# Kernel optimization log

Measured on AMD Instinct MI355X. Metric: run time of the kernel, lower is better.

The kernel has to match this reference:

```python
import jax, jax.numpy as jnp
import numpy as np

B, S, E, H = 4, 2048, 1024, 16
D = E // H  # per-head dim
SCALE = float(1.0 / np.sqrt(D))


def setup_inputs() -> dict:
    key = jax.random.key(0)
    k1, k2, k3 = jax.random.split(key, 3)
    x = jax.random.normal(k1, (B, S, E), dtype=jnp.float32)
    # xavier_uniform for torch Linear weights (shape [out, in])
    lim_qkv = float(np.sqrt(6.0 / (E + 3 * E)))
    w_qkv = jax.random.uniform(k2, (3 * E, E), minval=-lim_qkv, maxval=lim_qkv, dtype=jnp.float32)
    lim_o = float(np.sqrt(6.0 / (E + E)))
    w_o = jax.random.uniform(k3, (E, E), minval=-lim_o, maxval=lim_o, dtype=jnp.float32)
    return {"x": x, "w_qkv": w_qkv, "w_o": w_o}


def reference(x, w_qkv, w_o):
    b, s, e = x.shape
    # self-attention projection: (b,s,3E) -> (b,s,H,3D) -> chunk into q,k,v
    qkv = (x @ w_qkv.T).reshape(b, s, H, 3 * D)
    q, k, v = jnp.split(qkv, 3, axis=-1)           # each (b,s,H,D)
    q = q.transpose(0, 2, 1, 3)                    # (b,H,s,D)
    k = k.transpose(0, 2, 1, 3)
    v = v.transpose(0, 2, 1, 3)
    logits = jnp.einsum("bhsd,bhtd->bhst", q, k) * SCALE  # (b,H,s,s)
    # NOTE: faithful to source bug — values use raw scaled logits, not softmax(logits)
    values = jnp.einsum("bhst,bhtd->bhsd", logits, v)     # (b,H,s,D)
    values = values.transpose(0, 2, 1, 3).reshape(b, s, e)
    return values @ w_o.T
```

## Files before the change

kernel.cpp:

```cpp
#include <hip/hip_runtime.h>
#include <hip/hip_bf16.h>
#include <cstdint>

#define SCALE_F 0.125f

typedef __attribute__((ext_vector_type(8))) short bf16x8;
typedef __attribute__((ext_vector_type(4))) float f32x4;
typedef __attribute__((ext_vector_type(4))) unsigned short u16x4;
typedef __attribute__((ext_vector_type(8))) unsigned short u16x8;

typedef const __attribute__((address_space(1))) void glb_void;
typedef __attribute__((address_space(3))) void lds_void;

static __device__ __forceinline__ unsigned short f2bf(float f) {
  unsigned u = __builtin_bit_cast(unsigned, f);
  u = (u + 0x7fffu + ((u >> 16) & 1u)) >> 16;
  return (unsigned short)u;
}
static __device__ __forceinline__ float bf2f(unsigned short s) {
  unsigned u = ((unsigned)s) << 16;
  return __builtin_bit_cast(float, u);
}

static __device__ __forceinline__ int xcd_work(int bid, int nwg) {
  int cpx = nwg >> 3;
  return (bid & 7) * cpx + (bid >> 3);
}

__global__ __launch_bounds__(256) void prep(const float* __restrict__ x,
                                            const float* __restrict__ wqkv,
                                            const float* __restrict__ wo,
                                            unsigned short* __restrict__ xb,
                                            unsigned short* __restrict__ xT,
                                            unsigned short* __restrict__ wqt,
                                            unsigned short* __restrict__ wk,
                                            unsigned short* __restrict__ wv,
                                            unsigned short* __restrict__ wob) {
  __shared__ unsigned short lds[64][72];
  const int t = threadIdx.x;
  const int bid = blockIdx.x;

  if (bid < 2048) {
    const int r0 = (bid & 127) * 64, c0 = (bid >> 7) * 64;
#pragma unroll
    for (int pass = 0; pass < 4; ++pass) {
      int r = pass * 16 + (t >> 4);
      int c = (t & 15) * 4;
      float4 v = *(const float4*)(x + (size_t)(r0 + r) * 1024 + c0 + c);
      u16x4 o = { f2bf(v.x), f2bf(v.y), f2bf(v.z), f2bf(v.w) };
      *(u16x4*)(xb + (size_t)(r0 + r) * 1024 + c0 + c) = o;
#pragma unroll
      for (int j = 0; j < 4; ++j) {
        int C = c + j;
        lds[C][r ^ ((C & 7) << 3)] = o[j];
      }
    }
    __syncthreads();
#pragma unroll
    for (int pass = 0; pass < 2; ++pass) {
      int rr = pass * 32 + (t >> 3);
      int cc = (t & 7) * 8;
      u16x8 v = *(const u16x8*)&lds[rr][cc ^ ((rr & 7) << 3)];
      *(u16x8*)(xT + (size_t)(c0 + rr) * 8192 + r0 + cc) = v;
    }
  } else if (bid < 5120) {
    int row = bid - 2048;
    const float* src;
    unsigned short* dst;
    if (row < 1024) {
      int h = row >> 6, k = row & 63;
      src = wqkv + (size_t)(h * 192 + 64 + k) * 1024;
      dst = wk + (size_t)row * 1024;
    } else if (row < 2048) {
      int local = row - 1024;
      int h = local >> 6, k = local & 63;
      src = wqkv + (size_t)(h * 192 + 128 + k) * 1024;
      dst = wv + (size_t)local * 1024;
    } else {
      int local = row - 2048;
      src = wo + (size_t)local * 1024;
      dst = wob + (size_t)local * 1024;
    }
    float4 v = *(const float4*)(src + t * 4);
    u16x4 o = { f2bf(v.x), f2bf(v.y), f2bf(v.z), f2bf(v.w) };
    *(u16x4*)(dst + t * 4) = o;
  } else {
    int tid = bid - 5120;
    const int r0 = (tid & 15) * 64, c0 = (tid >> 4) * 64;
#pragma unroll
    for (int pass = 0; pass < 4; ++pass) {
      int r = pass * 16 + (t >> 4);
      int c = (t & 15) * 4;
      int gr = r0 + r;
      int srcRow = (gr >> 6) * 192 + (gr & 63);
      float4 v = *(const float4*)(wqkv + (size_t)srcRow * 1024 + c0 + c);
      lds[c + 0][r] = f2bf(v.x);
      lds[c + 1][r] = f2bf(v.y);
      lds[c + 2][r] = f2bf(v.z);
      lds[c + 3][r] = f2bf(v.w);
    }
    __syncthreads();
#pragma unroll
    for (int pass = 0; pass < 2; ++pass) {
      int rr = pass * 32 + (t >> 3);
      int cc = (t & 7) * 8;
      *(u16x8*)(wqt + (size_t)(c0 + rr) * 1024 + r0 + cc) = *(const u16x8*)&lds[rr][cc];
    }
  }
}

template<bool F32OUT>
__global__ __launch_bounds__(512) void gemm_bt(const unsigned short* __restrict__ A, int lda,
                                               long aB, long aP,
                                               const unsigned short* __restrict__ Bm, int ldb,
                                               long bB, long bP,
                                               void* __restrict__ Cv, int ldc,
                                               long cB, long cP,
                                               int K, int psplit, int nx, int ny) {
  __shared__ __align__(16) unsigned short Ash[2][128 * 32];
  __shared__ __align__(16) unsigned short Bsh[2][128 * 32];
  const int work = xcd_work(blockIdx.x, gridDim.x);
  const int xt = work % nx;
  const int yt = (work / nx) % ny;
  const int z  = work / (nx * ny);
  const int bb = z / psplit, pp = z % psplit;
  A  += (size_t)bb * aB + (size_t)pp * aP;
  Bm += (size_t)bb * bB + (size_t)pp * bP;
  const int t = threadIdx.x;
  const int w = t >> 6, l = t & 63;
  const int lr = l & 15, lk = l >> 4;
  const int m0 = yt * 128, n0 = xt * 128;
  const int wr = (w >> 2) * 64, wc = (w & 3) * 32;
  const int srow = t >> 2;
  const int skc = ((t & 3) ^ ((srow >> 1) & 3)) << 3;
  const size_t aOff = (size_t)(m0 + srow) * lda + skc;
  const size_t bOff = (size_t)(n0 + srow) * ldb + skc;
  const int fxor = ((lk ^ ((lr >> 1) & 3)) << 3);
  f32x4 acc[4][2] = {};

  __builtin_amdgcn_global_load_lds((glb_void*)(A + aOff), (lds_void*)(Ash[0] + w * 512), 16, 0, 0);
  __builtin_amdgcn_global_load_lds((glb_void*)(Bm + bOff), (lds_void*)(Bsh[0] + w * 512), 16, 0, 0);
  __syncthreads();

  int cur = 0;
  for (int k0 = 0; k0 < K; k0 += 32, cur ^= 1) {
    if (k0 + 32 < K) {
      __builtin_amdgcn_global_load_lds((glb_void*)(A + aOff + k0 + 32),
                                       (lds_void*)(Ash[cur ^ 1] + w * 512), 16, 0, 0);
      __builtin_amdgcn_global_load_lds((glb_void*)(Bm + bOff + k0 + 32),
                                       (lds_void*)(Bsh[cur ^ 1] + w * 512), 16, 0, 0);
    }
    bf16x8 af[4], bfv[2];
#pragma unroll
    for (int mi = 0; mi < 4; ++mi)
      af[mi] = *(const bf16x8*)(Ash[cur] + (wr + mi * 16 + lr) * 32 + fxor);
#pragma unroll
    for (int ni = 0; ni < 2; ++ni)
      bfv[ni] = *(const bf16x8*)(Bsh[cur] + (wc + ni * 16 + lr) * 32 + fxor);
#pragma unroll
    for (int mi = 0; mi < 4; ++mi)
#pragma unroll
      for (int ni = 0; ni < 2; ++ni)
        acc[mi][ni] = __builtin_amdgcn_mfma_f32_16x16x32_bf16(af[mi], bfv[ni], acc[mi][ni], 0, 0, 0);
    __syncthreads();
  }

#pragma unroll
  for (int mi = 0; mi < 4; ++mi)
#pragma unroll
    for (int ni = 0; ni < 2; ++ni)
#pragma unroll
      for (int r = 0; r < 4; ++r) {
        const size_t row = (size_t)(m0 + wr + mi * 16 + lk * 4 + r);
        const size_t col = (size_t)(n0 + wc + ni * 16 + lr);
        if constexpr (F32OUT)
          ((float*)Cv)[(size_t)bb * cB + (size_t)pp * cP + row * ldc + col] = acc[mi][ni][r];
        else
          ((unsigned short*)Cv)[(size_t)bb * cB + (size_t)pp * cP + row * ldc + col] = f2bf(acc[mi][ni][r]);
      }
}

__global__ __launch_bounds__(512) void gemm_tri(const unsigned short* __restrict__ xT,
                                                unsigned short* __restrict__ Gp) {
  __shared__ __align__(16) unsigned short Ash[2][128 * 32];
  __shared__ __align__(16) unsigned short Bsh[2][128 * 32];
  const int work = xcd_work(blockIdx.x, gridDim.x);
  int ti = work % 36;
  const int z = work / 36;
  int mt = 0, accum = 0;
  while (accum + mt + 1 <= ti) { accum += mt + 1; ++mt; }
  int nt = ti - accum;
  const int b = z >> 2, p = z & 3;
  const unsigned short* base = xT + (size_t)b * 2048 + (size_t)p * 512;

  const int t = threadIdx.x;
  const int w = t >> 6, l = t & 63;
  const int lr = l & 15, lk = l >> 4;
  const int m0 = mt * 128, n0 = nt * 128;
  const int wr = (w >> 2) * 64, wc = (w & 3) * 32;
  const int srow = t >> 2;
  const int skc = ((t & 3) ^ ((srow >> 1) & 3)) << 3;
  const size_t aOff = (size_t)(m0 + srow) * 8192 + skc;
  const size_t bOff = (size_t)(n0 + srow) * 8192 + skc;
  const int fxor = ((lk ^ ((lr >> 1) & 3)) << 3);
  f32x4 acc[4][2] = {};

  __builtin_amdgcn_global_load_lds((glb_void*)(base + aOff), (lds_void*)(Ash[0] + w * 512), 16, 0, 0);
  __builtin_amdgcn_global_load_lds((glb_void*)(base + bOff), (lds_void*)(Bsh[0] + w * 512), 16, 0, 0);
  __syncthreads();

  int cur = 0;
  for (int k0 = 0; k0 < 512; k0 += 32, cur ^= 1) {
    if (k0 + 32 < 512) {
      __builtin_amdgcn_global_load_lds((glb_void*)(base + aOff + k0 + 32),
                                       (lds_void*)(Ash[cur ^ 1] + w * 512), 16, 0, 0);
      __builtin_amdgcn_global_load_lds((glb_void*)(base + bOff + k0 + 32),
                                       (lds_void*)(Bsh[cur ^ 1] + w * 512), 16, 0, 0);
    }
    bf16x8 af[4], bfv[2];
#pragma unroll
    for (int mi = 0; mi < 4; ++mi)
      af[mi] = *(const bf16x8*)(Ash[cur] + (wr + mi * 16 + lr) * 32 + fxor);
#pragma unroll
    for (int ni = 0; ni < 2; ++ni)
      bfv[ni] = *(const bf16x8*)(Bsh[cur] + (wc + ni * 16 + lr) * 32 + fxor);
#pragma unroll
    for (int mi = 0; mi < 4; ++mi)
#pragma unroll
      for (int ni = 0; ni < 2; ++ni)
        acc[mi][ni] = __builtin_amdgcn_mfma_f32_16x16x32_bf16(af[mi], bfv[ni], acc[mi][ni], 0, 0, 0);
    __syncthreads();
  }

  unsigned short* out = Gp + (size_t)z * 1048576;
#pragma unroll
  for (int mi = 0; mi < 4; ++mi)
#pragma unroll
    for (int ni = 0; ni < 2; ++ni)
#pragma unroll
      for (int r = 0; r < 4; ++r)
        out[(size_t)(m0 + wr + mi * 16 + lk * 4 + r) * 1024 + n0 + wc + ni * 16 + lr]
            = f2bf(acc[mi][ni][r]);
}

__global__ __launch_bounds__(256) void mirror_reduce(const unsigned short* __restrict__ Gp,
                                                     unsigned short* __restrict__ G) {
  __shared__ unsigned short ldsT[128][128];
  int ti = blockIdx.x;
  int mt = 0, accum = 0;
  while (accum + mt + 1 <= ti) { accum += mt + 1; ++mt; }
  int nt = ti - accum;
  const int b = blockIdx.y;
  const int m0 = mt * 128, n0 = nt * 128;
  const unsigned short* base = Gp + (size_t)b * 4 * 1048576;
  unsigned short* Gb = G + (size_t)b * 1048576;
  const int t = threadIdx.x;

#pragma unroll
  for (int pass = 0; pass < 8; ++pass) {
    int idx = pass * 2048 + t * 8;
    int r = idx >> 7, c = idx & 127;
    float s[8] = {};
#pragma unroll
    for (int p = 0; p < 4; ++p) {
      u16x8 v = *(const u16x8*)(base + (size_t)p * 1048576 + (size_t)(m0 + r) * 1024 + n0 + c);
#pragma unroll
      for (int j = 0; j < 8; ++j) s[j] += bf2f(v[j]);
    }
    u16x8 o;
#pragma unroll
    for (int j = 0; j < 8; ++j) o[j] = f2bf(s[j]);
    *(u16x8*)(Gb + (size_t)(m0 + r) * 1024 + n0 + c) = o;
#pragma unroll
    for (int j = 0; j < 8; ++j) {
      int col = c + j;
      ldsT[col][r ^ (((col >> 3) & 7) << 3)] = o[j];
    }
  }

  if (mt != nt) {
    __syncthreads();
#pragma unroll
    for (int pass = 0; pass < 8; ++pass) {
      int idx = pass * 2048 + t * 8;
      int rr = idx >> 7, cc = idx & 127;
      u16x8 v = *(const u16x8*)&ldsT[rr][cc ^ (((rr >> 3) & 7) << 3)];
      *(u16x8*)(Gb + (size_t)(n0 + rr) * 1024 + m0 + cc) = v;
    }
  }
}

__global__ __launch_bounds__(512) void mdirect(const unsigned short* __restrict__ wk,
                                               const unsigned short* __restrict__ G,
                                               const unsigned short* __restrict__ wv,
                                               float* __restrict__ Mp) {
  __shared__ __align__(16) unsigned short Awk[2][64 * 32];
  __shared__ __align__(16) unsigned short Bg[2][128 * 32];
  __shared__ __align__(16) unsigned short Ut[64 * 128];
  __shared__ __align__(16) unsigned short WvS[64 * 128];
  const int work = xcd_work(blockIdx.x, gridDim.x);
  const int bh = work >> 3, es = work & 7;
  const int b = bh >> 4, h = bh & 15;
  const int e0 = es * 128;
  const int t = threadIdx.x;
  const int w = t >> 6, l = t & 63;
  const int lr = l & 15, lk = l >> 4;

  const unsigned short* wkB = wk + (size_t)(h * 64) * 1024;
  const unsigned short* Gb  = G + (size_t)b * 1048576 + (size_t)e0 * 1024;
  const unsigned short* wvB = wv + (size_t)(h * 64) * 1024 + e0;

  const int arow = t >> 2, askc = ((t & 3) ^ ((arow >> 1) & 3)) << 3;
  const int brow = t >> 2, bskc = ((t & 3) ^ ((brow >> 1) & 3)) << 3;
  const size_t aOff = (size_t)arow * 1024 + askc;
  const size_t bOff = (size_t)brow * 1024 + bskc;
  const int fxor = ((lk ^ ((lr >> 1) & 3)) << 3);

#pragma unroll
  for (int i = 0; i < 2; ++i) {
    int idx = i * 512 + t;
    int row = idx >> 4, slot = idx & 15;
    int sslot = slot ^ (row & 15);
    __builtin_amdgcn_global_load_lds(
        (glb_void*)(wvB + (size_t)row * 1024 + sslot * 8),
        (lds_void*)(WvS + i * 4096 + w * 512), 16, 0, 0);
  }
  if (t < 256)
    __builtin_amdgcn_global_load_lds((glb_void*)(wkB + aOff),
                                     (lds_void*)(Awk[0] + w * 512), 16, 0, 0);
  __builtin_amdgcn_global_load_lds((glb_void*)(Gb + bOff),
                                   (lds_void*)(Bg[0] + w * 512), 16, 0, 0);
  __syncthreads();

  const int wc = w * 16;
  f32x4 acc[4] = {};
  int cur = 0;
  for (int k0 = 0; k0 < 1024; k0 += 32, cur ^= 1) {
    if (k0 + 32 < 1024) {
      if (t < 256)
        __builtin_amdgcn_global_load_lds((glb_void*)(wkB + aOff + k0 + 32),
                                         (lds_void*)(Awk[cur ^ 1] + w * 512), 16, 0, 0);
      __builtin_amdgcn_global_load_lds((glb_void*)(Gb + bOff + k0 + 32),
                                       (lds_void*)(Bg[cur ^ 1] + w * 512), 16, 0, 0);
    }
    bf16x8 af[4], bfv;
#pragma unroll
    for (int mi = 0; mi < 4; ++mi)
      af[mi] = *(const bf16x8*)(Awk[cur] + (mi * 16 + lr) * 32 + fxor);
    bfv = *(const bf16x8*)(Bg[cur] + (wc + lr) * 32 + fxor);
#pragma unroll
    for (int mi = 0; mi < 4; ++mi)
      acc[mi] = __builtin_amdgcn_mfma_f32_16x16x32_bf16(af[mi], bfv, acc[mi], 0, 0, 0);
    __syncthreads();
  }

#pragma unroll
  for (int mi = 0; mi < 4; ++mi)
#pragma unroll
    for (int r = 0; r < 4; ++r) {
      int i = mi * 16 + lk * 4 + r;
      int col = wc + lr;
      int addr = i * 128 + ((((col >> 3) ^ (i & 15)) << 3) | (col & 7));
      Ut[addr] = f2bf(acc[mi][r]);
    }
  __syncthreads();

  if (w < 4) {
    f32x4 acc2[4] = {};
#pragma unroll
    for (int ks = 0; ks < 4; ++ks) {
      int slot = (ks << 2) | lk;
      bf16x8 a2 = *(const bf16x8*)(Ut + (w * 16 + lr) * 128 + ((slot ^ lr) << 3));
      bf16x8 b2[4];
#pragma unroll
      for (int ni = 0; ni < 4; ++ni)
        b2[ni] = *(const bf16x8*)(WvS + (ni * 16 + lr) * 128 + ((slot ^ lr) << 3));
#pragma unroll
      for (int ni = 0; ni < 4; ++ni)
        acc2[ni] = __builtin_amdgcn_mfma_f32_16x16x32_bf16(a2, b2[ni], acc2[ni], 0, 0, 0);
    }
    float* out = Mp + ((size_t)bh * 8 + es) * 4096;
#pragma unroll
    for (int ni = 0; ni < 4; ++ni)
#pragma unroll
      for (int r = 0; r < 4; ++r)
        out[(w * 16 + lk * 4 + r) * 64 + ni * 16 + lr] = acc2[ni][r];
  }
}

__global__ __launch_bounds__(256) void amat_fused(const float* __restrict__ Mp,
                                                  const unsigned short* __restrict__ wqt,
                                                  unsigned short* __restrict__ Amat) {
  __shared__ float Msh[64 * 68];
  __shared__ unsigned short MtSh[64][80];
  const int t = threadIdx.x;
  const int et = blockIdx.x, bh = blockIdx.y;
  const int b = bh >> 4, h = bh & 15;

  const float* base = Mp + (size_t)bh * 32768;
  for (int i = t * 4; i < 4096; i += 1024) {
    float4 s = *(const float4*)(base + i);
#pragma unroll
    for (int p = 1; p < 8; ++p) {
      float4 v = *(const float4*)(base + p * 4096 + i);
      s.x += v.x; s.y += v.y; s.z += v.z; s.w += v.w;
    }
    int k = i >> 6, dp = i & 63;
    *(float4*)&Msh[k * 68 + dp] = s;
  }
  __syncthreads();

  for (int i = t; i < 4096; i += 256) {
    int dp = i >> 6, k = i & 63;
    MtSh[dp][k] = f2bf(Msh[k * 68 + dp] * SCALE_F);
  }
  __syncthreads();

  const int w = t >> 6, l = t & 63;
  const int lr = l & 15, lk = l >> 4;
  const int e0 = et * 128 + w * 32;

  f32x4 acc[2][4] = {};
#pragma unroll
  for (int ks = 0; ks < 2; ++ks) {
    bf16x8 af[2], bfv[4];
#pragma unroll
    for (int mi = 0; mi < 2; ++mi)
      af[mi] = *(const bf16x8*)(wqt + (size_t)(e0 + mi * 16 + lr) * 1024 + h * 64 + ks * 32 + lk * 8);
#pragma unroll
    for (int ni = 0; ni < 4; ++ni)
      bfv[ni] = *(const bf16x8*)(&MtSh[ni * 16 + lr][ks * 32 + lk * 8]);
#pragma unroll
    for (int mi = 0; mi < 2; ++mi)
#pragma unroll
      for (int ni = 0; ni < 4; ++ni)
        acc[mi][ni] = __builtin_amdgcn_mfma_f32_16x16x32_bf16(af[mi], bfv[ni], acc[mi][ni], 0, 0, 0);
  }
#pragma unroll
  for (int mi = 0; mi < 2; ++mi)
#pragma unroll
    for (int ni = 0; ni < 4; ++ni)
#pragma unroll
      for (int r = 0; r < 4; ++r)
        Amat[(size_t)b * 1048576 + (size_t)(e0 + mi * 16 + lk * 4 + r) * 1024 + h * 64 + ni * 16 + lr]
            = f2bf(acc[mi][ni][r]);
}

extern "C" void kernel_launch(void* const* d_in, const int* in_sizes, int n_in,
                              void* d_out, int out_size, void* d_ws, size_t ws_size,
                              hipStream_t stream) {
  const float* x    = (const float*)d_in[0];
  const float* wqkv = (const float*)d_in[1];
  const float* wo   = (const float*)d_in[2];
  float* out = (float*)d_out;

  char* ws = (char*)d_ws;
  const size_t MB = 1048576;
  unsigned short* xb   = (unsigned short*)(ws + 0);
  unsigned short* xT   = (unsigned short*)(ws + 16 * MB);
  unsigned short* wqt  = (unsigned short*)(ws + 32 * MB);
  unsigned short* wk   = (unsigned short*)(ws + 34 * MB);
  unsigned short* wv   = (unsigned short*)(ws + 36 * MB);
  unsigned short* wob  = (unsigned short*)(ws + 38 * MB);
  unsigned short* Gp   = (unsigned short*)(ws + 40 * MB);
  unsigned short* G    = (unsigned short*)(ws + 72 * MB);
  float*          Mp   = (float*)        (ws + 40 * MB);
  unsigned short* Amat = (unsigned short*)(ws + 48 * MB);
  unsigned short* Weff = (unsigned short*)(ws + 56 * MB);

  const long M1 = 1048576;

  prep<<<5376, 256, 0, stream>>>(x, wqkv, wo, xb, xT, wqt, wk, wv, wob);

  gemm_tri<<<576, 512, 0, stream>>>(xT, Gp);
  mirror_reduce<<<dim3(36, 4), 256, 0, stream>>>(Gp, G);

  mdirect<<<512, 512, 0, stream>>>(wk, G, wv, Mp);

  amat_fused<<<dim3(8, 64), 256, 0, stream>>>(Mp, wqt, Amat);

  gemm_bt<false><<<256, 512, 0, stream>>>(wob, 1024, 0, 0,
                                          Amat, 1024, M1, 0,
                                          (void*)Weff, 1024, M1, 0, 1024, 1, 8, 8);

  gemm_bt<true><<<512, 512, 0, stream>>>(xb, 1024, 2048 * 1024L, 0,
                                         Weff, 1024, M1, 0,
                                         (void*)out, 1024, 2048 * 1024L, 0, 1024, 1, 8, 16);
}
```

Before: 122.6 us.

## Fuse weight conversion into mirror-reduce, retile Gram and output GEMMs

The x conversion now runs in its own prep kernel. The weight bf16 conversions are moved into the mirror_reduce launch, so they run after the Gram GEMM and the separate reduce launch goes away. gemm_tri switches to 256 threads with a 64x64 tile per wave, which gives more MFMA work per LDS fragment load. The final output GEMM is replaced by a dedicated 128x256-tile kernel, which raises data reuse but yields fewer, larger workgroups (256), and that may leave some CUs idle.

```diff
diff --git a/kernel.cpp b/kernel.cpp
--- a/kernel.cpp
+++ b/kernel.cpp
@@ -27,44 +27,92 @@
   return (bid & 7) * cpx + (bid >> 3);
 }
 
-__global__ __launch_bounds__(256) void prep(const float* __restrict__ x,
-                                            const float* __restrict__ wqkv,
-                                            const float* __restrict__ wo,
-                                            unsigned short* __restrict__ xb,
-                                            unsigned short* __restrict__ xT,
-                                            unsigned short* __restrict__ wqt,
-                                            unsigned short* __restrict__ wk,
-                                            unsigned short* __restrict__ wv,
-                                            unsigned short* __restrict__ wob) {
+__global__ __launch_bounds__(256) void prep_x(const float* __restrict__ x,
+                                              unsigned short* __restrict__ xb,
+                                              unsigned short* __restrict__ xT) {
   __shared__ unsigned short lds[64][72];
   const int t = threadIdx.x;
   const int bid = blockIdx.x;
-
-  if (bid < 2048) {
-    const int r0 = (bid & 127) * 64, c0 = (bid >> 7) * 64;
-#pragma unroll
-    for (int pass = 0; pass < 4; ++pass) {
-      int r = pass * 16 + (t >> 4);
-      int c = (t & 15) * 4;
-      float4 v = *(const float4*)(x + (size_t)(r0 + r) * 1024 + c0 + c);
-      u16x4 o = { f2bf(v.x), f2bf(v.y), f2bf(v.z), f2bf(v.w) };
-      *(u16x4*)(xb + (size_t)(r0 + r) * 1024 + c0 + c) = o;
-#pragma unroll
-      for (int j = 0; j < 4; ++j) {
-        int C = c + j;
-        lds[C][r ^ ((C & 7) << 3)] = o[j];
+  const int r0 = (bid & 127) * 64, c0 = (bid >> 7) * 64;
+#pragma unroll
+  for (int pass = 0; pass < 4; ++pass) {
+    int r = pass * 16 + (t >> 4);
+    int c = (t & 15) * 4;
+    float4 v = *(const float4*)(x + (size_t)(r0 + r) * 1024 + c0 + c);
+    u16x4 o = { f2bf(v.x), f2bf(v.y), f2bf(v.z), f2bf(v.w) };
+    *(u16x4*)(xb + (size_t)(r0 + r) * 1024 + c0 + c) = o;
+#pragma unroll
+    for (int j = 0; j < 4; ++j) {
+      int C = c + j;
+      lds[C][r ^ ((C & 7) << 3)] = o[j];
+    }
+  }
+  __syncthreads();
+#pragma unroll
+  for (int pass = 0; pass < 2; ++pass) {
+    int rr = pass * 32 + (t >> 3);
+    int cc = (t & 7) * 8;
+    u16x8 v = *(const u16x8*)&lds[rr][cc ^ ((rr & 7) << 3)];
+    *(u16x8*)(xT + (size_t)(c0 + rr) * 8192 + r0 + cc) = v;
+  }
+}
+
+__global__ __launch_bounds__(256) void mirror_w(const unsigned short* __restrict__ Gp,
+                                                unsigned short* __restrict__ G,
+                                                const float* __restrict__ wqkv,
+                                                const float* __restrict__ wo,
+                                                unsigned short* __restrict__ wqt,
+                                                unsigned short* __restrict__ wk,
+                                                unsigned short* __restrict__ wv,
+                                                unsigned short* __restrict__ wob) {
+  __shared__ unsigned short ldsT[128][128];
+  __shared__ unsigned short lds[64][72];
+  const int t = threadIdx.x;
+  const int bid = blockIdx.x;
+
+  if (bid < 144) {
+    int ti = bid % 36;
+    const int b = bid / 36;
+    int mt = 0, accum = 0;
+    while (accum + mt + 1 <= ti) { accum += mt + 1; ++mt; }
+    int nt = ti - accum;
+    const int m0 = mt * 128, n0 = nt * 128;
+    const unsigned short* base = Gp + (size_t)b * 4 * 1048576;
+    unsigned short* Gb = G + (size_t)b * 1048576;
+
+#pragma unroll
+    for (int pass = 0; pass < 8; ++pass) {
+      int idx = pass * 2048 + t * 8;
+      int r = idx >> 7, c = idx & 127;
+      float s[8] = {};
+#pragma unroll
+      for (int p = 0; p < 4; ++p) {
+        u16x8 v = *(const u16x8*)(base + (size_t)p * 1048576 + (size_t)(m0 + r) * 1024 + n0 + c);
+#pragma unroll
+        for (int j = 0; j < 8; ++j) s[j] += bf2f(v[j]);
       }
-    }
-    __syncthreads();
-#pragma unroll
-    for (int pass = 0; pass < 2; ++pass) {
-      int rr = pass * 32 + (t >> 3);
-      int cc = (t & 7) * 8;
-      u16x8 v = *(const u16x8*)&lds[rr][cc ^ ((rr & 7) << 3)];
-      *(u16x8*)(xT + (size_t)(c0 + rr) * 8192 + r0 + cc) = v;
-    }
-  } else if (bid < 5120) {
-    int row = bid - 2048;
+      u16x8 o;
+#pragma unroll
+      for (int j = 0; j < 8; ++j) o[j] = f2bf(s[j]);
+      *(u16x8*)(Gb + (size_t)(m0 + r) * 1024 + n0 + c) = o;
+#pragma unroll
+      for (int j = 0; j < 8; ++j) {
+        int col = c + j;
+        ldsT[col][r ^ (((col >> 3) & 7) << 3)] = o[j];
+      }
+    }
+    if (mt != nt) {
+      __syncthreads();
+#pragma unroll
+      for (int pass = 0; pass < 8; ++pass) {
+        int idx = pass * 2048 + t * 8;
+        int rr = idx >> 7, cc = idx & 127;
+        u16x8 v = *(const u16x8*)&ldsT[rr][cc ^ (((rr >> 3) & 7) << 3)];
+        *(u16x8*)(Gb + (size_t)(n0 + rr) * 1024 + m0 + cc) = v;
+      }
+    }
+  } else if (bid < 3216) {
+    int row = bid - 144;
     const float* src;
     unsigned short* dst;
     if (row < 1024) {
@@ -85,7 +133,7 @@
     u16x4 o = { f2bf(v.x), f2bf(v.y), f2bf(v.z), f2bf(v.w) };
     *(u16x4*)(dst + t * 4) = o;
   } else {
-    int tid = bid - 5120;
+    int tid = bid - 3216;
     const int r0 = (tid & 15) * 64, c0 = (tid >> 4) * 64;
 #pragma unroll
     for (int pass = 0; pass < 4; ++pass) {
@@ -180,7 +228,71 @@
       }
 }
 
-__global__ __launch_bounds__(512) void gemm_tri(const unsigned short* __restrict__ xT,
+__global__ __launch_bounds__(512) void gemm_out(const unsigned short* __restrict__ xb,
+                                                const unsigned short* __restrict__ Weff,
+                                                float* __restrict__ outp) {
+  __shared__ __align__(16) unsigned short Ash[2][128 * 32];
+  __shared__ __align__(16) unsigned short Bsh[2][256 * 32];
+  const int work = xcd_work(blockIdx.x, gridDim.x);
+  const int xt = work & 3;
+  const int yt = (work >> 2) & 15;
+  const int z  = work >> 6;
+  const unsigned short* A  = xb + (size_t)z * 2048 * 1024;
+  const unsigned short* Bm = Weff + (size_t)z * 1048576;
+  float* C = outp + (size_t)z * 2048 * 1024;
+  const int t = threadIdx.x;
+  const int w = t >> 6, l = t & 63;
+  const int lr = l & 15, lk = l >> 4;
+  const int m0 = yt * 128, n0 = xt * 256;
+  const int wr = (w >> 2) * 64, wc = (w & 3) * 64;
+  const int srow = t >> 2;
+  const int skc = ((t & 3) ^ ((srow >> 1) & 3)) << 3;
+  const size_t aOff  = (size_t)(m0 + srow) * 1024 + skc;
+  const size_t b0Off = (size_t)(n0 + srow) * 1024 + skc;
+  const size_t b1Off = (size_t)(n0 + 128 + srow) * 1024 + skc;
+  const int fxor = ((lk ^ ((lr >> 1) & 3)) << 3);
+  f32x4 acc[4][4] = {};
+
+  __builtin_amdgcn_global_load_lds((glb_void*)(A + aOff),   (lds_void*)(Ash[0] + w * 512), 16, 0, 0);
+  __builtin_amdgcn_global_load_lds((glb_void*)(Bm + b0Off), (lds_void*)(Bsh[0] + w * 512), 16, 0, 0);
+  __builtin_amdgcn_global_load_lds((glb_void*)(Bm + b1Off), (lds_void*)(Bsh[0] + 4096 + w * 512), 16, 0, 0);
+  __syncthreads();
+
+  int cur = 0;
+  for (int k0 = 0; k0 < 1024; k0 += 32, cur ^= 1) {
+    if (k0 + 32 < 1024) {
+      __builtin_amdgcn_global_load_lds((glb_void*)(A + aOff + k0 + 32),
+                                       (lds_void*)(Ash[cur ^ 1] + w * 512), 16, 0, 0);
+      __builtin_amdgcn_global_load_lds((glb_void*)(Bm + b0Off + k0 + 32),
+                                       (lds_void*)(Bsh[cur ^ 1] + w * 512), 16, 0, 0);
+      __builtin_amdgcn_global_load_lds((glb_void*)(Bm + b1Off + k0 + 32),
+                                       (lds_void*)(Bsh[cur ^ 1] + 4096 + w * 512), 16, 0, 0);
+    }
+    bf16x8 af[4], bfv[4];
+#pragma unroll
+    for (int mi = 0; mi < 4; ++mi)
+      af[mi] = *(const bf16x8*)(Ash[cur] + (wr + mi * 16 + lr) * 32 + fxor);
+#pragma unroll
+    for (int ni = 0; ni < 4; ++ni)
+      bfv[ni] = *(const bf16x8*)(Bsh[cur] + (wc + ni * 16 + lr) * 32 + fxor);
+#pragma unroll
+    for (int mi = 0; mi < 4; ++mi)
+#pragma unroll
+      for (int ni = 0; ni < 4; ++ni)
+        acc[mi][ni] = __builtin_amdgcn_mfma_f32_16x16x32_bf16(af[mi], bfv[ni], acc[mi][ni], 0, 0, 0);
+    __syncthreads();
+  }
+
+#pragma unroll
+  for (int mi = 0; mi < 4; ++mi)
+#pragma unroll
+    for (int ni = 0; ni < 4; ++ni)
+#pragma unroll
+      for (int r = 0; r < 4; ++r)
+        C[(size_t)(m0 + wr + mi * 16 + lk * 4 + r) * 1024 + n0 + wc + ni * 16 + lr] = acc[mi][ni][r];
+}
+
+__global__ __launch_bounds__(256) void gemm_tri(const unsigned short* __restrict__ xT,
                                                 unsigned short* __restrict__ Gp) {
   __shared__ __align__(16) unsigned short Ash[2][128 * 32];
   __shared__ __align__(16) unsigned short Bsh[2][128 * 32];
@@ -197,97 +309,58 @@
   const int w = t >> 6, l = t & 63;
   const int lr = l & 15, lk = l >> 4;
   const int m0 = mt * 128, n0 = nt * 128;
-  const int wr = (w >> 2) * 64, wc = (w & 3) * 32;
-  const int srow = t >> 2;
-  const int skc = ((t & 3) ^ ((srow >> 1) & 3)) << 3;
-  const size_t aOff = (size_t)(m0 + srow) * 8192 + skc;
-  const size_t bOff = (size_t)(n0 + srow) * 8192 + skc;
+  const int wr = (w >> 1) * 64, wc = (w & 1) * 64;
+  const int c0i = t, c1i = 256 + t;
+  const int r0s = c0i >> 2, r1s = c1i >> 2;
+  const int s0 = ((c0i & 3) ^ ((r0s >> 1) & 3)) << 3;
+  const int s1 = ((c1i & 3) ^ ((r1s >> 1) & 3)) << 3;
+  const size_t a0 = (size_t)(m0 + r0s) * 8192 + s0, a1 = (size_t)(m0 + r1s) * 8192 + s1;
+  const size_t b0 = (size_t)(n0 + r0s) * 8192 + s0, b1 = (size_t)(n0 + r1s) * 8192 + s1;
   const int fxor = ((lk ^ ((lr >> 1) & 3)) << 3);
-  f32x4 acc[4][2] = {};
-
-  __builtin_amdgcn_global_load_lds((glb_void*)(base + aOff), (lds_void*)(Ash[0] + w * 512), 16, 0, 0);
-  __builtin_amdgcn_global_load_lds((glb_void*)(base + bOff), (lds_void*)(Bsh[0] + w * 512), 16, 0, 0);
+  f32x4 acc[4][4] = {};
+
+  __builtin_amdgcn_global_load_lds((glb_void*)(base + a0), (lds_void*)(Ash[0] + w * 512), 16, 0, 0);
+  __builtin_amdgcn_global_load_lds((glb_void*)(base + a1), (lds_void*)(Ash[0] + 2048 + w * 512), 16, 0, 0);
+  __builtin_amdgcn_global_load_lds((glb_void*)(base + b0), (lds_void*)(Bsh[0] + w * 512), 16, 0, 0);
+  __builtin_amdgcn_global_load_lds((glb_void*)(base + b1), (lds_void*)(Bsh[0] + 2048 + w * 512), 16, 0, 0);
   __syncthreads();
 
   int cur = 0;
   for (int k0 = 0; k0 < 512; k0 += 32, cur ^= 1) {
     if (k0 + 32 < 512) {
-      __builtin_amdgcn_global_load_lds((glb_void*)(base + aOff + k0 + 32),
+      __builtin_amdgcn_global_load_lds((glb_void*)(base + a0 + k0 + 32),
                                        (lds_void*)(Ash[cur ^ 1] + w * 512), 16, 0, 0);
-      __builtin_amdgcn_global_load_lds((glb_void*)(base + bOff + k0 + 32),
+      __builtin_amdgcn_global_load_lds((glb_void*)(base + a1 + k0 + 32),
+                                       (lds_void*)(Ash[cur ^ 1] + 2048 + w * 512), 16, 0, 0);
+      __builtin_amdgcn_global_load_lds((glb_void*)(base + b0 + k0 + 32),
                                        (lds_void*)(Bsh[cur ^ 1] + w * 512), 16, 0, 0);
-    }
-    bf16x8 af[4], bfv[2];
+      __builtin_amdgcn_global_load_lds((glb_void*)(base + b1 + k0 + 32),
+                                       (lds_void*)(Bsh[cur ^ 1] + 2048 + w * 512), 16, 0, 0);
+    }
+    bf16x8 af[4], bfv[4];
 #pragma unroll
     for (int mi = 0; mi < 4; ++mi)
       af[mi] = *(const bf16x8*)(Ash[cur] + (wr + mi * 16 + lr) * 32 + fxor);
 #pragma unroll
-    for (int ni = 0; ni < 2; ++ni)
+    for (int ni = 0; ni < 4; ++ni)
       bfv[ni] = *(const bf16x8*)(Bsh[cur] + (wc + ni * 16 + lr) * 32 + fxor);
 #pragma unroll
     for (int mi = 0; mi < 4; ++mi)
 #pragma unroll
-      for (int ni = 0; ni < 2; ++ni)
+      for (int ni = 0; ni < 4; ++ni)
         acc[mi][ni] = __builtin_amdgcn_mfma_f32_16x16x32_bf16(af[mi], bfv[ni], acc[mi][ni], 0, 0, 0);
     __syncthreads();
   }
 
-  unsigned short* out = Gp + (size_t)z * 1048576;
+  unsigned short* outb = Gp + (size_t)z * 1048576;
 #pragma unroll
   for (int mi = 0; mi < 4; ++mi)
 #pragma unroll
-    for (int ni = 0; ni < 2; ++ni)
+    for (int ni = 0; ni < 4; ++ni)
 #pragma unroll
       for (int r = 0; r < 4; ++r)
-        out[(size_t)(m0 + wr + mi * 16 + lk * 4 + r) * 1024 + n0 + wc + ni * 16 + lr]
+        outb[(size_t)(m0 + wr + mi * 16 + lk * 4 + r) * 1024 + n0 + wc + ni * 16 + lr]
             = f2bf(acc[mi][ni][r]);
-}
-
-__global__ __launch_bounds__(256) void mirror_reduce(const unsigned short* __restrict__ Gp,
-                                                     unsigned short* __restrict__ G) {
-  __shared__ unsigned short ldsT[128][128];
-  int ti = blockIdx.x;
-  int mt = 0, accum = 0;
-  while (accum + mt + 1 <= ti) { accum += mt + 1; ++mt; }
-  int nt = ti - accum;
-  const int b = blockIdx.y;
-  const int m0 = mt * 128, n0 = nt * 128;
-  const unsigned short* base = Gp + (size_t)b * 4 * 1048576;
-  unsigned short* Gb = G + (size_t)b * 1048576;
-  const int t = threadIdx.x;
-
-#pragma unroll
-  for (int pass = 0; pass < 8; ++pass) {
-    int idx = pass * 2048 + t * 8;
-    int r = idx >> 7, c = idx & 127;
-    float s[8] = {};
-#pragma unroll
-    for (int p = 0; p < 4; ++p) {
-      u16x8 v = *(const u16x8*)(base + (size_t)p * 1048576 + (size_t)(m0 + r) * 1024 + n0 + c);
-#pragma unroll
-      for (int j = 0; j < 8; ++j) s[j] += bf2f(v[j]);
-    }
-    u16x8 o;
-#pragma unroll
-    for (int j = 0; j < 8; ++j) o[j] = f2bf(s[j]);
-    *(u16x8*)(Gb + (size_t)(m0 + r) * 1024 + n0 + c) = o;
-#pragma unroll
-    for (int j = 0; j < 8; ++j) {
-      int col = c + j;
-      ldsT[col][r ^ (((col >> 3) & 7) << 3)] = o[j];
-    }
-  }
-
-  if (mt != nt) {
-    __syncthreads();
-#pragma unroll
-    for (int pass = 0; pass < 8; ++pass) {
-      int idx = pass * 2048 + t * 8;
-      int rr = idx >> 7, cc = idx & 127;
-      u16x8 v = *(const u16x8*)&ldsT[rr][cc ^ (((rr >> 3) & 7) << 3)];
-      *(u16x8*)(Gb + (size_t)(n0 + rr) * 1024 + m0 + cc) = v;
-    }
-  }
 }
 
 __global__ __launch_bounds__(512) void mdirect(const unsigned short* __restrict__ wk,
@@ -379,12 +452,12 @@
       for (int ni = 0; ni < 4; ++ni)
         acc2[ni] = __builtin_amdgcn_mfma_f32_16x16x32_bf16(a2, b2[ni], acc2[ni], 0, 0, 0);
     }
-    float* out = Mp + ((size_t)bh * 8 + es) * 4096;
+    float* outp = Mp + ((size_t)bh * 8 + es) * 4096;
 #pragma unroll
     for (int ni = 0; ni < 4; ++ni)
 #pragma unroll
       for (int r = 0; r < 4; ++r)
-        out[(w * 16 + lk * 4 + r) * 64 + ni * 16 + lr] = acc2[ni][r];
+        outp[(w * 16 + lk * 4 + r) * 64 + ni * 16 + lr] = acc2[ni][r];
   }
 }
 
@@ -470,10 +543,11 @@
 
   const long M1 = 1048576;
 
-  prep<<<5376, 256, 0, stream>>>(x, wqkv, wo, xb, xT, wqt, wk, wv, wob);
-
-  gemm_tri<<<576, 512, 0, stream>>>(xT, Gp);
-  mirror_reduce<<<dim3(36, 4), 256, 0, stream>>>(Gp, G);
+  prep_x<<<2048, 256, 0, stream>>>(x, xb, xT);
+
+  gemm_tri<<<576, 256, 0, stream>>>(xT, Gp);
+
+  mirror_w<<<3472, 256, 0, stream>>>(Gp, G, wqkv, wo, wqt, wk, wv, wob);
 
   mdirect<<<512, 512, 0, stream>>>(wk, G, wv, Mp);
 
@@ -483,7 +557,5 @@
                                           Amat, 1024, M1, 0,
                                           (void*)Weff, 1024, M1, 0, 1024, 1, 8, 8);
 
-  gemm_bt<true><<<512, 512, 0, stream>>>(xb, 1024, 2048 * 1024L, 0,
-                                         Weff, 1024, M1, 0,
-                                         (void*)out, 1024, 2048 * 1024L, 0, 1024, 1, 8, 16);
-}
+  gemm_out<<<256, 512, 0, stream>>>(xb, Weff, out);
+}
```

Measured after the change: 122.8 us. No clear change (+0.2%).
